# Optimization experiments

Measured on AMD Instinct MI355X. Metric: run time of the kernel, lower is better.

Reference implementation:

```python
import jax, jax.numpy as jnp
import numpy as np
import math

B, S, D = 16, 577, 768          # batch, seq (24*24 grid + 1 cls), in_dim=att_dim
H, HD = 12, 64                  # heads, head_dim
GRID = 24                       # height = width; S = GRID*GRID + rpe_skip
RATIO = 1.9
ALPHA, BETA, GAMMA = 1.0 * RATIO, 2.0 * RATIO, 8.0 * RATIO
BETA_INT = int(BETA)            # 3
NUM_BUCKETS = (2 * BETA_INT + 1) ** 2 + 1  # 49 product buckets + 1 extra for skip (cls) = 50


def _piecewise_index(d):
    # iRPE piecewise bucket index (numpy, static). d: integer offsets.
    d = d.astype(np.float64)
    ad = np.abs(d)
    log_part = ALPHA + np.log(np.maximum(ad, 1e-9) / ALPHA) / math.log(GAMMA / ALPHA) * (BETA - ALPHA)
    y_out = np.sign(d) * np.clip(np.round(log_part), None, BETA)
    idx = np.where(ad <= ALPHA, np.round(d), y_out)
    return np.trunc(idx).astype(np.int64)  # torch .to(int) truncates toward zero


def make_rp_bucket():
    # 2D 'product' method bucket ids with skip=1 (cls token -> extra bucket)
    ii, jj = np.meshgrid(np.arange(GRID), np.arange(GRID), indexing='ij')
    pos = np.stack([ii.ravel(), jj.ravel()], axis=-1)          # (L,2)
    diff = pos[:, None, :] - pos[None, :, :]                    # (L,L,2)
    Sb = 2 * BETA_INT + 1
    r = _piecewise_index(diff[..., 0]) + BETA_INT               # [0, 2*beta_int]
    c = _piecewise_index(diff[..., 1]) + BETA_INT
    pid = r * Sb + c                                            # [0, 48]
    L = GRID * GRID
    bucket = np.full((L + 1, L + 1), NUM_BUCKETS - 1, dtype=np.int32)
    bucket[1:, 1:] = pid
    return jnp.asarray(bucket)


def setup_inputs() -> dict:
    key = jax.random.key(0)
    k1, k2, k3 = jax.random.split(key, 3)
    x = jax.random.normal(k1, (B, S, D), dtype=jnp.float32)
    w_qkv = jax.random.normal(k2, (3 * D, D), dtype=jnp.float32) * 0.02   # torch Linear weight (out,in)
    rpe_table = jax.random.normal(k3, (HD, NUM_BUCKETS), dtype=jnp.float32) * 0.02  # shared-head contextual table
    rp_bucket = make_rp_bucket()                                # (S,S) int32
    return {"x": x, "w_qkv": w_qkv, "rpe_table": rpe_table, "rp_bucket": rp_bucket}


def reference(x, w_qkv, rpe_table, rp_bucket):
    qkv = x @ w_qkv.T                                           # (B,S,3D)
    q, k, v = jnp.split(qkv, 3, axis=-1)
    # Faithful to torch source: plain reshape (B,S,D)->(B,H,S,HD) (no transpose-split)
    scale = 1.0 / jnp.sqrt(jnp.asarray(HD, x.dtype))
    q = q.reshape(B, H, S, HD) * scale
    k = k.reshape(B, H, S, HD)
    v = v.reshape(B, H, S, HD)
    qk = jnp.einsum('bhid,bhjd->bhij', q, k)                    # (B,H,S,S)
    # contextual rpe_k: bias[b,h,i,j] = (q[b,h,i] . rpe_table[:, rp_bucket[i,j]])
    ctx = jnp.einsum('bhid,dc->bhic', q, rpe_table)             # (B,H,S,NUM_BUCKETS)
    idx = jnp.broadcast_to(rp_bucket[None, None].astype(jnp.int32), (B, H, S, S))
    bias = jnp.take_along_axis(ctx, idx, axis=-1)               # (B,H,S,S)
    att = jax.nn.softmax(qk + bias, axis=-1)
    out = jnp.einsum('bhij,bhjd->bhid', att, v)                 # (B,H,S,HD)
    y = out.transpose(0, 2, 1, 3).reshape(B, S, D)              # out_proj is Identity (out_dim==att_dim)
    return y
```

## Files before the change

kernel.cpp:

```cpp
#include <hip/hip_runtime.h>

constexpr int BN_  = 16;
constexpr int SN_  = 577;
constexpr int SP_  = 640;
constexpr int DN_  = 768;
constexpr int HN_  = 12;
constexpr int HD_  = 64;
constexpr int NB_  = 50;
constexpr int MR_  = BN_ * SN_;
constexpr int MRP_ = 73 * 128;
constexpr int NQ_  = 3 * DN_;
constexpr int BHS_ = BN_ * HN_ * SN_;
constexpr int SHD_ = SN_ * HD_;

typedef __attribute__((ext_vector_type(8))) short short8;
typedef __attribute__((ext_vector_type(4))) float f32x4;

__device__ __forceinline__ short f2bf(float f) {
  union { float f; unsigned u; } v; v.f = f;
  unsigned r = (v.u + 0x7fffu + ((v.u >> 16) & 1u)) >> 16;
  return (short)r;
}

__device__ __forceinline__ float ex2(float x) {
  float r; asm("v_exp_f32 %0, %1" : "=v"(r) : "v"(x)); return r;
}

__device__ __forceinline__ unsigned cvtpk(float a, float b) {
  unsigned r; asm("v_cvt_pk_bf16_f32 %0, %1, %2" : "=v"(r) : "v"(a), "v"(b));
  return r;
}

__device__ __forceinline__ float bf2f(unsigned short u) {
  union { unsigned u; float f; } v; v.u = ((unsigned)u) << 16; return v.f;
}

__device__ __forceinline__ void gload16(const void* g, void* l) {
  __builtin_amdgcn_global_load_lds(
      (const __attribute__((address_space(1))) unsigned int*)g,
      (__attribute__((address_space(3))) unsigned int*)l, 16, 0, 0);
}

__launch_bounds__(256)
__global__ void cvt_k(const float* __restrict__ src, short* __restrict__ dst,
                      int n_src, int n_dst) {
  const int i = (blockIdx.x * 256 + threadIdx.x) * 8;
  if (i >= n_dst) return;
  union { short8 v; short u[8]; } pk;
  if (i < n_src) {
    const float4 a = *(const float4*)(src + i);
    const float4 b = *(const float4*)(src + i + 4);
    pk.u[0] = f2bf(a.x); pk.u[1] = f2bf(a.y); pk.u[2] = f2bf(a.z); pk.u[3] = f2bf(a.w);
    pk.u[4] = f2bf(b.x); pk.u[5] = f2bf(b.y); pk.u[6] = f2bf(b.z); pk.u[7] = f2bf(b.w);
  } else {
#pragma unroll
    for (int j = 0; j < 8; ++j) pk.u[j] = 0;
  }
  *(short8*)(dst + i) = pk.v;
}

__launch_bounds__(256)
__global__ void rpb8_k(const int* __restrict__ rpb, unsigned char* __restrict__ rpbu8) {
  const int tid = blockIdx.x * 256 + threadIdx.x;
  if (tid >= SN_ * 160) return;
  const int i = tid / 160, c4 = tid - i * 160;
  const int j = c4 * 4;
  uchar4 o;
  o.x = (j     < SN_) ? (unsigned char)rpb[i * SN_ + j    ] : 0;
  o.y = (j + 1 < SN_) ? (unsigned char)rpb[i * SN_ + j + 1] : 0;
  o.z = (j + 2 < SN_) ? (unsigned char)rpb[i * SN_ + j + 2] : 0;
  o.w = (j + 3 < SN_) ? (unsigned char)rpb[i * SN_ + j + 3] : 0;
  *(uchar4*)(rpbu8 + (size_t)i * 640 + j) = o;
}

__launch_bounds__(256)
__global__ void qkv_mfma_k(const short* __restrict__ xb, const short* __restrict__ wb,
                           short* __restrict__ Qbf, short* __restrict__ Ksw,
                           short* __restrict__ Vbf) {
  __shared__ short At[128 * 64];
  __shared__ short Bt[128 * 64];
  const int t = threadIdx.x;
  const int w = t >> 6, lane = t & 63, g = lane >> 4, ln = lane & 15;
  const int wm = w >> 1, wn = w & 1;
  const int m0 = blockIdx.y * 128, n0 = blockIdx.x * 128;

  const int rlo = lane >> 3;
  const int gu  = (lane & 7) ^ rlo;
  const short* ga[4]; const short* gb[4];
  short* la[4]; short* lb[4];
#pragma unroll
  for (int q = 0; q < 4; ++q) {
    const int rl = w * 32 + q * 8 + rlo;
    ga[q] = xb + (size_t)(m0 + rl) * DN_ + gu * 8;
    gb[q] = wb + (size_t)(n0 + rl) * DN_ + gu * 8;
    la[q] = At + w * 2048 + q * 512;
    lb[q] = Bt + w * 2048 + q * 512;
  }

  f32x4 acc[4][4];
#pragma unroll
  for (int mt = 0; mt < 4; ++mt)
#pragma unroll
    for (int nt = 0; nt < 4; ++nt) acc[mt][nt] = (f32x4){0.f, 0.f, 0.f, 0.f};

  for (int k0 = 0; k0 < DN_; k0 += 64) {
    __syncthreads();
#pragma unroll
    for (int q = 0; q < 4; ++q) {
      gload16(ga[q] + k0, la[q]);
      gload16(gb[q] + k0, lb[q]);
    }
    __syncthreads();
#pragma unroll
    for (int kc = 0; kc < 2; ++kc) {
      short8 af[4], bf[4];
#pragma unroll
      for (int mt = 0; mt < 4; ++mt) {
        const int row = wm * 64 + mt * 16 + ln;
        const int u = (kc * 4 + g) ^ (row & 7);
        af[mt] = *(const short8*)&At[row * 64 + u * 8];
      }
#pragma unroll
      for (int nt = 0; nt < 4; ++nt) {
        const int row = wn * 64 + nt * 16 + ln;
        const int u = (kc * 4 + g) ^ (row & 7);
        bf[nt] = *(const short8*)&Bt[row * 64 + u * 8];
      }
#pragma unroll
      for (int mt = 0; mt < 4; ++mt)
#pragma unroll
        for (int nt = 0; nt < 4; ++nt)
          acc[mt][nt] = __builtin_amdgcn_mfma_f32_16x16x32_bf16(af[mt], bf[nt], acc[mt][nt], 0, 0, 0);
    }
  }

  const int nw0  = n0 + wn * 64;
  const int secg = nw0 / DN_;
  const int cbw  = nw0 - secg * DN_;
  const float QSC = 0.18033688011112042f;
#pragma unroll
  for (int mt = 0; mt < 4; ++mt) {
#pragma unroll
    for (int r = 0; r < 4; ++r) {
      const int gm = m0 + wm * 64 + mt * 16 + 4 * g + r;
      if (gm >= MR_) continue;
      const int bb = gm / SN_;
      const int ss = gm - bb * SN_;
      const int pb = ss * DN_ + cbw;
#pragma unroll
      for (int nt = 0; nt < 4; ++nt) {
        const int p   = pb + nt * 16 + ln;
        const int hh  = p / SHD_;
        const int rem = p - hh * SHD_;
        const int ii  = rem >> 6;
        const int dd  = rem & 63;
        const size_t ro = (size_t)(bb * HN_ + hh);
        const float v = acc[mt][nt][r];
        if (secg == 0) {
          Qbf[(ro * SN_ + ii) * 64 + dd] = f2bf(v * QSC);
        } else if (secg == 1) {
          Ksw[(ro * SP_ + ii) * 64 + (dd ^ ((ii & 7) << 3))] = f2bf(v);
        } else {
          Vbf[(ro * SP_ + ii) * 64 + dd] = f2bf(v);
        }
      }
    }
  }
}

__launch_bounds__(256)
__global__ void vtr_k(const short* __restrict__ Vbf, short* __restrict__ Vtsw) {
  __shared__ short T[64][72];
  const int t = threadIdx.x;
  const int jt = blockIdx.x, bh = blockIdx.y;
  const int j0 = jt * 64;
  {
    const int r = t >> 2, c0 = (t & 3) * 16;
    const short* src = Vbf + ((size_t)bh * SP_ + j0 + r) * 64 + c0;
    *(short8*)&T[r][c0]     = *(const short8*)(src);
    *(short8*)&T[r][c0 + 8] = *(const short8*)(src + 8);
  }
  __syncthreads();
  const int d = t >> 2;
  short* dst = Vtsw + ((size_t)bh * 64 + d) * SP_;
  const int sw = (d & 7) << 3;
#pragma unroll
  for (int e = 0; e < 4; ++e) {
    const int jl = (t & 3) * 16 + e * 4;
    const int jg = j0 + jl;
    short4 v;
    v.x = (jg + 0 < SN_) ? T[jl + 0][d] : (short)0;
    v.y = (jg + 1 < SN_) ? T[jl + 1][d] : (short)0;
    v.z = (jg + 2 < SN_) ? T[jl + 2][d] : (short)0;
    v.w = (jg + 3 < SN_) ? T[jl + 3][d] : (short)0;
    const int oq = (jg >> 2) & 7;
    const int pq = ((oq & 3) << 1) | (oq >> 2);
    const int p  = (jg & ~31) | (pq << 2);
    *(short4*)&dst[p ^ sw] = v;
  }
}

__launch_bounds__(256)
__global__ void attn_k(const short* __restrict__ Qbf, const short* __restrict__ Ksw,
                       const short* __restrict__ Vtsw, const float* __restrict__ rpe,
                       const unsigned char* __restrict__ rpbu8, float* __restrict__ y) {
  __shared__ short Kt[4096];
  __shared__ short Vt[4096];
  __shared__ unsigned char rpbt[128 * 68];
  __shared__ unsigned short ctxs[4][32][53];
  short (*Rp)[64] = (short (*)[64])rpbt;

  const int t = threadIdx.x;
  const int w = t >> 6, lane = t & 63, g = lane >> 4, ln = lane & 15;
  const int wg = blockIdx.x;
  const int xcd = wg & 7, idx = wg >> 3;
  const int qt = idx % 5;
  const int bh = (idx / 5) * 8 + xcd;
  const int b = bh / HN_, h = bh - b * HN_;
  const int i0 = qt * 128;
  const size_t rb = (size_t)bh * SN_;
  const short* Kbh = Ksw + (size_t)bh * SP_ * 64;
  const short* Vbh = Vtsw + (size_t)bh * 64 * SP_;

  const int tK = t * 8;
  const int vRow = t >> 3, vCol = (t & 7) * 8;
  const int rpRow = t >> 1, rpCol = (t & 1) * 32;
  const int irow_s = (i0 + rpRow <= SN_ - 1) ? (i0 + rpRow) : (SN_ - 1);

  short8 kr0, kr1, vr0, vr1; int4 rp0_, rp1_;
  kr0 = *(const short8*)(Kbh + tK);
  kr1 = *(const short8*)(Kbh + 2048 + tK);
  vr0 = *(const short8*)(Vbh + (size_t)vRow * SP_ + vCol);
  vr1 = *(const short8*)(Vbh + (size_t)(32 + vRow) * SP_ + vCol);
  rp0_ = *(const int4*)(rpbu8 + (size_t)irow_s * 640 + rpCol);
  rp1_ = *(const int4*)(rpbu8 + (size_t)irow_s * 640 + rpCol + 16);

  for (int e = t; e < 64 * 64; e += 256) {
    const int c = e >> 6, d = e & 63;
    Rp[c][d] = (c < NB_) ? f2bf(rpe[d * NB_ + c]) : (short)0;
  }

  short8 qf[2][2];
#pragma unroll
  for (int s = 0; s < 2; ++s) {
    int row = i0 + 32 * w + 16 * s + ln; if (row > SN_ - 1) row = SN_ - 1;
    const short* qp = Qbf + (rb + row) * 64;
    qf[s][0] = *(const short8*)(qp + 8 * g);
    qf[s][1] = *(const short8*)(qp + 32 + 8 * g);
  }

  __syncthreads();

  {
    f32x4 accC[2][4];
#pragma unroll
    for (int s = 0; s < 2; ++s)
#pragma unroll
      for (int ct = 0; ct < 4; ++ct) accC[s][ct] = (f32x4){0.f, 0.f, 0.f, 0.f};
#pragma unroll
    for (int kc = 0; kc < 2; ++kc) {
#pragma unroll
      for (int ct = 0; ct < 4; ++ct) {
        const short8 rf = *(const short8*)&Rp[ct * 16 + ln][kc * 32 + 8 * g];
        accC[0][ct] = __builtin_amdgcn_mfma_f32_16x16x32_bf16(qf[0][kc], rf, accC[0][ct], 0, 0, 0);
        accC[1][ct] = __builtin_amdgcn_mfma_f32_16x16x32_bf16(qf[1][kc], rf, accC[1][ct], 0, 0, 0);
      }
    }
#pragma unroll
    for (int s = 0; s < 2; ++s)
#pragma unroll
      for (int ct = 0; ct < 4; ++ct) {
        const int c = ct * 16 + ln;
        if (c < 53) {
#pragma unroll
          for (int r = 0; r < 4; ++r)
            ctxs[w][16 * s + 4 * g + r][c] = (unsigned short)f2bf(accC[s][ct][r]);
        }
      }
  }

  float m0s = -3e38f, m1s = -3e38f, l0s = 0.f, l1s = 0.f;
  f32x4 accO[2][4];
#pragma unroll
  for (int s = 0; s < 2; ++s)
#pragma unroll
    for (int dt = 0; dt < 4; ++dt) accO[s][dt] = (f32x4){0.f, 0.f, 0.f, 0.f};

  const int swv = (ln & 7) << 3;

  for (int jt = 0; jt < 10; ++jt) {
    __syncthreads();
    *(short8*)&Kt[tK]        = kr0;
    *(short8*)&Kt[2048 + tK] = kr1;
    *(short8*)&Vt[tK]        = vr0;
    *(short8*)&Vt[2048 + tK] = vr1;
    *(int4*)&rpbt[rpRow * 68 + rpCol]      = rp0_;
    *(int4*)&rpbt[rpRow * 68 + rpCol + 16] = rp1_;
    __syncthreads();

    if (jt < 9) {
      const int jn = jt * 64 + 64;
      kr0 = *(const short8*)(Kbh + (size_t)jn * 64 + tK);
      kr1 = *(const short8*)(Kbh + (size_t)jn * 64 + 2048 + tK);
      vr0 = *(const short8*)(Vbh + (size_t)vRow * SP_ + jn + vCol);
      vr1 = *(const short8*)(Vbh + (size_t)(32 + vRow) * SP_ + jn + vCol);
      rp0_ = *(const int4*)(rpbu8 + (size_t)irow_s * 640 + jn + rpCol);
      rp1_ = *(const int4*)(rpbu8 + (size_t)irow_s * 640 + jn + rpCol + 16);
    }

    f32x4 accS[2][4];
#pragma unroll
    for (int s = 0; s < 2; ++s)
#pragma unroll
      for (int nt = 0; nt < 4; ++nt) accS[s][nt] = (f32x4){0.f, 0.f, 0.f, 0.f};
    __builtin_amdgcn_s_setprio(1);
#pragma unroll
    for (int kc = 0; kc < 2; ++kc) {
      const int cb = (kc * 32 + 8 * g) ^ swv;
#pragma unroll
      for (int nt = 0; nt < 4; ++nt) {
        const short8 kf = *(const short8*)&Kt[(nt * 16 + ln) * 64 + cb];
        accS[0][nt] = __builtin_amdgcn_mfma_f32_16x16x32_bf16(kf, qf[0][kc], accS[0][nt], 0, 0, 0);
        accS[1][nt] = __builtin_amdgcn_mfma_f32_16x16x32_bf16(kf, qf[1][kc], accS[1][nt], 0, 0, 0);
      }
    }
    __builtin_amdgcn_s_setprio(0);

    short8 pf[2][2];
#pragma unroll
    for (int s = 0; s < 2; ++s) {
      const unsigned short* cbase = &ctxs[w][16 * s + ln][0];
      const int rpoff = (32 * w + 16 * s + ln) * 68;
      float pv[4][4];
#pragma unroll
      for (int nt = 0; nt < 4; ++nt) {
        const uchar4 bk = *(const uchar4*)&rpbt[rpoff + nt * 16 + 4 * g];
        pv[nt][0] = accS[s][nt][0] + bf2f(cbase[bk.x]);
        pv[nt][1] = accS[s][nt][1] + bf2f(cbase[bk.y]);
        pv[nt][2] = accS[s][nt][2] + bf2f(cbase[bk.z]);
        pv[nt][3] = accS[s][nt][3] + bf2f(cbase[bk.w]);
      }
      if (jt == 9) {
#pragma unroll
        for (int nt = 0; nt < 4; ++nt) {
          const int jb = jt * 64 + nt * 16 + 4 * g;
#pragma unroll
          for (int r = 0; r < 4; ++r)
            if (jb + r >= SN_) pv[nt][r] = -3e38f;
        }
      }

      float& m = (s == 0) ? m0s : m1s;
      float& l = (s == 0) ? l0s : l1s;

      float mq[4];
#pragma unroll
      for (int nt = 0; nt < 4; ++nt)
        mq[nt] = fmaxf(fmaxf(pv[nt][0], pv[nt][1]), fmaxf(pv[nt][2], pv[nt][3]));
      float mx = fmaxf(fmaxf(mq[0], mq[1]), fmaxf(mq[2], mq[3]));
      mx = fmaxf(mx, __shfl_xor(mx, 16));
      mx = fmaxf(mx, __shfl_xor(mx, 32));

      if (__any(mx > m + 8.f)) {
        const float mnew = fmaxf(m, mx);
        const float sc = ex2(m - mnew);
        float scr[4];
#pragma unroll
        for (int r = 0; r < 4; ++r) scr[r] = __shfl(sc, 4 * g + r);
#pragma unroll
        for (int dt = 0; dt < 4; ++dt)
#pragma unroll
          for (int r = 0; r < 4; ++r) accO[s][dt][r] *= scr[r];
        l *= sc;
        m = mnew;
      }

#pragma unroll
      for (int nt = 0; nt < 4; ++nt)
#pragma unroll
        for (int r = 0; r < 4; ++r)
          pv[nt][r] = ex2(pv[nt][r] - m);
      float sq[4];
#pragma unroll
      for (int nt = 0; nt < 4; ++nt)
        sq[nt] = (pv[nt][0] + pv[nt][1]) + (pv[nt][2] + pv[nt][3]);
      float sum = (sq[0] + sq[1]) + (sq[2] + sq[3]);
      sum += __shfl_xor(sum, 16);
      sum += __shfl_xor(sum, 32);
      l += sum;

#pragma unroll
      for (int kc = 0; kc < 2; ++kc) {
        union { short8 v; unsigned wd[4]; } pk;
        pk.wd[0] = cvtpk(pv[2 * kc][0],     pv[2 * kc][1]);
        pk.wd[1] = cvtpk(pv[2 * kc][2],     pv[2 * kc][3]);
        pk.wd[2] = cvtpk(pv[2 * kc + 1][0], pv[2 * kc + 1][1]);
        pk.wd[3] = cvtpk(pv[2 * kc + 1][2], pv[2 * kc + 1][3]);
        pf[s][kc] = pk.v;
      }
    }

    __builtin_amdgcn_s_setprio(1);
#pragma unroll
    for (int kc = 0; kc < 2; ++kc) {
      const int cb = (kc * 32 + 8 * g) ^ swv;
#pragma unroll
      for (int dt = 0; dt < 4; ++dt) {
        const short8 vf = *(const short8*)&Vt[(dt * 16 + ln) * 64 + cb];
        accO[0][dt] = __builtin_amdgcn_mfma_f32_16x16x32_bf16(pf[0][kc], vf, accO[0][dt], 0, 0, 0);
        accO[1][dt] = __builtin_amdgcn_mfma_f32_16x16x32_bf16(pf[1][kc], vf, accO[1][dt], 0, 0, 0);
      }
    }
    __builtin_amdgcn_s_setprio(0);
  }

#pragma unroll
  for (int s = 0; s < 2; ++s) {
    const float lv = (s == 0) ? l0s : l1s;
    float linv[4];
#pragma unroll
    for (int r = 0; r < 4; ++r) linv[r] = 1.f / __shfl(lv, 4 * g + r);
#pragma unroll
    for (int r = 0; r < 4; ++r) {
      const int i = i0 + 32 * w + 16 * s + 4 * g + r;
      if (i >= SN_) continue;
      float* yp = y + ((size_t)b * SN_ + i) * DN_ + h * HD_ + ln;
#pragma unroll
      for (int dt = 0; dt < 4; ++dt) yp[dt * 16] = accO[s][dt][r] * linv[r];
    }
  }
}

extern "C" void kernel_launch(void* const* d_in, const int* in_sizes, int n_in,
                              void* d_out, int out_size, void* d_ws, size_t ws_size,
                              hipStream_t stream) {
  const float* x   = (const float*)d_in[0];
  const float* w   = (const float*)d_in[1];
  const float* rpe = (const float*)d_in[2];
  const int*   rpb = (const int*)d_in[3];
  float* y = (float*)d_out;

  short* xb   = (short*)d_ws;
  short* wb   = xb + (size_t)MRP_ * DN_;
  short* Qbf  = wb + (size_t)NQ_ * DN_;
  short* Ksw  = Qbf + (size_t)BHS_ * HD_;
  short* Vbf  = Ksw + (size_t)BN_ * HN_ * SP_ * 64;
  short* Vtsw = Vbf + (size_t)BN_ * HN_ * SP_ * 64;
  unsigned char* rpbu8 = (unsigned char*)(Vtsw + (size_t)BN_ * HN_ * 64 * SP_);

  cvt_k<<<dim3(MRP_ * DN_ / 2048), 256, 0, stream>>>(x, xb, MR_ * DN_, MRP_ * DN_);
  cvt_k<<<dim3(NQ_ * DN_ / 2048), 256, 0, stream>>>(w, wb, NQ_ * DN_, NQ_ * DN_);
  rpb8_k<<<dim3((SN_ * 160 + 255) / 256), 256, 0, stream>>>(rpb, rpbu8);
  qkv_mfma_k<<<dim3(18, 73), 256, 0, stream>>>(xb, wb, Qbf, Ksw, Vbf);
  vtr_k<<<dim3(10, BN_ * HN_), 256, 0, stream>>>(Vbf, Vtsw);
  attn_k<<<dim3(960), 256, 0, stream>>>(Qbf, Ksw, Vtsw, rpe, rpbu8, y);
}
```

Baseline: 148.3 us.

## Double-buffer QKV GEMM LDS tiles and stage epilogue through LDS for vector stores

The QKV projection GEMM now uses two LDS buffers, prefetching the next K-slice while computing on the current one, which cuts one barrier per iteration. The epilogue writes the bf16 results into LDS per wave and then has each lane store a full 64-element row with 16-byte vector stores, replacing the scattered 2-byte global writes. LDS use grows to 64KB per block, which may lower occupancy. The staging also adds an extra LDS round trip per output.

```diff
diff --git a/kernel.cpp b/kernel.cpp
--- a/kernel.cpp
+++ b/kernel.cpp
@@ -77,8 +77,7 @@
 __global__ void qkv_mfma_k(const short* __restrict__ xb, const short* __restrict__ wb,
                            short* __restrict__ Qbf, short* __restrict__ Ksw,
                            short* __restrict__ Vbf) {
-  __shared__ short At[128 * 64];
-  __shared__ short Bt[128 * 64];
+  __shared__ short SB[32768];
   const int t = threadIdx.x;
   const int w = t >> 6, lane = t & 63, g = lane >> 4, ln = lane & 15;
   const int wm = w >> 1, wn = w & 1;
@@ -87,14 +86,13 @@
   const int rlo = lane >> 3;
   const int gu  = (lane & 7) ^ rlo;
   const short* ga[4]; const short* gb[4];
-  short* la[4]; short* lb[4];
+  int lOff[4];
 #pragma unroll
   for (int q = 0; q < 4; ++q) {
     const int rl = w * 32 + q * 8 + rlo;
     ga[q] = xb + (size_t)(m0 + rl) * DN_ + gu * 8;
     gb[q] = wb + (size_t)(n0 + rl) * DN_ + gu * 8;
-    la[q] = At + w * 2048 + q * 512;
-    lb[q] = Bt + w * 2048 + q * 512;
+    lOff[q] = w * 2048 + q * 512;
   }
 
   f32x4 acc[4][4];
@@ -103,14 +101,25 @@
 #pragma unroll
     for (int nt = 0; nt < 4; ++nt) acc[mt][nt] = (f32x4){0.f, 0.f, 0.f, 0.f};
 
+#pragma unroll
+  for (int q = 0; q < 4; ++q) {
+    gload16(ga[q], SB + lOff[q]);
+    gload16(gb[q], SB + 16384 + lOff[q]);
+  }
+  __syncthreads();
+
+  int cur = 0;
   for (int k0 = 0; k0 < DN_; k0 += 64) {
-    __syncthreads();
-#pragma unroll
-    for (int q = 0; q < 4; ++q) {
-      gload16(ga[q] + k0, la[q]);
-      gload16(gb[q] + k0, lb[q]);
-    }
-    __syncthreads();
+    if (k0 + 64 < DN_) {
+      const int nb = (cur ^ 1) * 8192;
+#pragma unroll
+      for (int q = 0; q < 4; ++q) {
+        gload16(ga[q] + k0 + 64, SB + nb + lOff[q]);
+        gload16(gb[q] + k0 + 64, SB + 16384 + nb + lOff[q]);
+      }
+    }
+    const short* Ac = SB + cur * 8192;
+    const short* Bc = SB + 16384 + cur * 8192;
 #pragma unroll
     for (int kc = 0; kc < 2; ++kc) {
       short8 af[4], bf[4];
@@ -118,13 +127,13 @@
       for (int mt = 0; mt < 4; ++mt) {
         const int row = wm * 64 + mt * 16 + ln;
         const int u = (kc * 4 + g) ^ (row & 7);
-        af[mt] = *(const short8*)&At[row * 64 + u * 8];
+        af[mt] = *(const short8*)&Ac[row * 64 + u * 8];
       }
 #pragma unroll
       for (int nt = 0; nt < 4; ++nt) {
         const int row = wn * 64 + nt * 16 + ln;
         const int u = (kc * 4 + g) ^ (row & 7);
-        bf[nt] = *(const short8*)&Bt[row * 64 + u * 8];
+        bf[nt] = *(const short8*)&Bc[row * 64 + u * 8];
       }
 #pragma unroll
       for (int mt = 0; mt < 4; ++mt)
@@ -132,38 +141,50 @@
         for (int nt = 0; nt < 4; ++nt)
           acc[mt][nt] = __builtin_amdgcn_mfma_f32_16x16x32_bf16(af[mt], bf[nt], acc[mt][nt], 0, 0, 0);
     }
-  }
-
+    __syncthreads();
+    cur ^= 1;
+  }
+
+  const int wbase = w * 4608;
   const int nw0  = n0 + wn * 64;
   const int secg = nw0 / DN_;
   const int cbw  = nw0 - secg * DN_;
   const float QSC = 0.18033688011112042f;
 #pragma unroll
-  for (int mt = 0; mt < 4; ++mt) {
-#pragma unroll
-    for (int r = 0; r < 4; ++r) {
-      const int gm = m0 + wm * 64 + mt * 16 + 4 * g + r;
-      if (gm >= MR_) continue;
-      const int bb = gm / SN_;
-      const int ss = gm - bb * SN_;
-      const int pb = ss * DN_ + cbw;
-#pragma unroll
-      for (int nt = 0; nt < 4; ++nt) {
-        const int p   = pb + nt * 16 + ln;
-        const int hh  = p / SHD_;
-        const int rem = p - hh * SHD_;
-        const int ii  = rem >> 6;
-        const int dd  = rem & 63;
-        const size_t ro = (size_t)(bb * HN_ + hh);
-        const float v = acc[mt][nt][r];
-        if (secg == 0) {
-          Qbf[(ro * SN_ + ii) * 64 + dd] = f2bf(v * QSC);
-        } else if (secg == 1) {
-          Ksw[(ro * SP_ + ii) * 64 + (dd ^ ((ii & 7) << 3))] = f2bf(v);
-        } else {
-          Vbf[(ro * SP_ + ii) * 64 + dd] = f2bf(v);
-        }
-      }
+  for (int mt = 0; mt < 4; ++mt)
+#pragma unroll
+    for (int nt = 0; nt < 4; ++nt)
+#pragma unroll
+      for (int r = 0; r < 4; ++r) {
+        float v = acc[mt][nt][r];
+        if (secg == 0) v *= QSC;
+        SB[wbase + (mt * 16 + 4 * g + r) * 72 + nt * 16 + ln] = f2bf(v);
+      }
+  const int gm = m0 + wm * 64 + lane;
+  if (gm < MR_) {
+    const int bb = gm / SN_;
+    const int ss = gm - bb * SN_;
+    const int pr = ss * DN_ + cbw;
+    const int hh = pr / SHD_;
+    const int ii = (pr - hh * SHD_) >> 6;
+    const size_t ro = (size_t)(bb * HN_ + hh);
+    const short* src = SB + wbase + lane * 72;
+    if (secg == 0) {
+      short* dst = Qbf + (ro * SN_ + ii) * 64;
+#pragma unroll
+      for (int u = 0; u < 8; ++u)
+        *(short8*)(dst + u * 8) = *(const short8*)(src + u * 8);
+    } else if (secg == 1) {
+      short* dst = Ksw + (ro * SP_ + ii) * 64;
+      const int sw = ii & 7;
+#pragma unroll
+      for (int u = 0; u < 8; ++u)
+        *(short8*)(dst + (u ^ sw) * 8) = *(const short8*)(src + u * 8);
+    } else {
+      short* dst = Vbf + (ro * SP_ + ii) * 64;
+#pragma unroll
+      for (int u = 0; u < 8; ++u)
+        *(short8*)(dst + u * 8) = *(const short8*)(src + u * 8);
     }
   }
 }
```

Result: faster. 143.9 us (-3.0%).
